# Performance work log

Hardware: AMD Instinct MI355X
Metric: run time of the kernel (lower is better)

Reference implementation:

```python
import jax, jax.numpy as jnp
import numpy as np

B, T, C, H = 4, 2048, 1024, 128

def setup_inputs() -> dict:
    key = jax.random.key(0)
    k1, k2, k3, k4 = jax.random.split(key, 4)
    x = jax.random.normal(k1, (B, T, C), dtype=jnp.float32)
    # nn.Linear(C, H, bias=False) weights, stored as [C, H] so y = x @ W
    scale = 1.0 / np.sqrt(C)
    Wq = jax.random.normal(k2, (C, H), dtype=jnp.float32) * scale
    Wk = jax.random.normal(k3, (C, H), dtype=jnp.float32) * scale
    Wv = jax.random.normal(k4, (C, H), dtype=jnp.float32) * scale
    mask = jnp.tril(jnp.ones((T, T), dtype=jnp.int32))  # causal mask
    return {"x": x, "Wq": Wq, "Wk": Wk, "Wv": Wv, "mask": mask}

def reference(x, Wq, Wk, Wv, mask):
    # x: [B,T,C]; projections to [B,T,H]
    q = jnp.einsum("btc,ch->bth", x, Wq)
    k = jnp.einsum("btc,ch->bth", x, Wk)
    v = jnp.einsum("btc,ch->bth", x, Wv)
    # NOTE: original scales by C**-0.5 (embedding dim), not head_size**-0.5
    inv_scale = x.shape[-1] ** (-0.5)
    scores = jnp.einsum("bth,bsh->bts", q, k) * inv_scale  # [B,T,T]
    scores = jnp.where(mask == 0, -jnp.inf, scores)
    weights = jax.nn.softmax(scores, axis=-1)
    # Dropout(0.1) is identity in eval mode
    return jnp.einsum("bts,bsh->bth", weights, v)  # [B,T,H]
```

## Files before the change

kernel.cpp:

```cpp
#include <hip/hip_runtime.h>
#include <hip/hip_bf16.h>
#include <cstdint>


typedef __bf16 bf16_t;
typedef __bf16 bf16x4 __attribute__((ext_vector_type(4)));
typedef __bf16 bf16x8 __attribute__((ext_vector_type(8)));
typedef float f32x4 __attribute__((ext_vector_type(4)));

#define MFMA16(a, b, c) __builtin_amdgcn_mfma_f32_16x16x32_bf16(a, b, c, 0, 0, 0)

constexpr int T = 2048;
constexpr int C = 1024;
constexpr int H = 128;

__device__ inline bf16x8 load8f(const float* __restrict__ p) {
    float4 a = *(const float4*)p;
    float4 b = *(const float4*)(p + 4);
    bf16x8 r;
    r[0] = (bf16_t)a.x; r[1] = (bf16_t)a.y; r[2] = (bf16_t)a.z; r[3] = (bf16_t)a.w;
    r[4] = (bf16_t)b.x; r[5] = (bf16_t)b.y; r[6] = (bf16_t)b.z; r[7] = (bf16_t)b.w;
    return r;
}

__global__ __launch_bounds__(256) void convert_x(const float* __restrict__ x,
                                                 bf16_t* __restrict__ xb, int n8) {
    int i = blockIdx.x * 256 + threadIdx.x;
    const int stride = gridDim.x * 256;
    for (; i < n8; i += stride)
        *(bf16x8*)(xb + (size_t)i * 8) = load8f(x + (size_t)i * 8);
}

__global__ void transpose_w(const float* __restrict__ Wq,
                            const float* __restrict__ Wk,
                            const float* __restrict__ Wv,
                            bf16_t* __restrict__ Wt) {
    __shared__ bf16_t tile[32][34];
    const float* W = blockIdx.z == 0 ? Wq : (blockIdx.z == 1 ? Wk : Wv);
    const int c0 = blockIdx.x * 32, h0 = blockIdx.y * 32;
    const int tx = threadIdx.x, ty = threadIdx.y;
#pragma unroll
    for (int i = 0; i < 4; i++)
        tile[ty + 8 * i][tx] = (bf16_t)W[(size_t)(c0 + ty + 8 * i) * H + h0 + tx];
    __syncthreads();
    bf16_t* Wtz = Wt + (size_t)blockIdx.z * H * C;
#pragma unroll
    for (int i = 0; i < 4; i++)
        Wtz[(size_t)(h0 + ty + 8 * i) * C + c0 + tx] = tile[tx][ty + 8 * i];
}

__global__ __launch_bounds__(256) void proj_gemm(const bf16_t* __restrict__ xb,
                                                 const bf16_t* __restrict__ Wt,
                                                 bf16_t* __restrict__ qout,
                                                 bf16_t* __restrict__ kout,
                                                 bf16_t* __restrict__ vtout) {
    const int w = threadIdx.x >> 6;
    const int wm = w & 1, wn = w >> 1;
    const int lane = threadIdx.x & 63;
    const int m16 = lane & 15, g = lane >> 4;
    const int z = blockIdx.z;
    const int m0 = blockIdx.x * 64 + wm * 32;
    const int n0 = blockIdx.y * 64 + wn * 32;

    const bf16_t* a0p = xb + (size_t)(m0 + m16) * C + g * 8;
    const bf16_t* a1p = a0p + (size_t)16 * C;
    const bf16_t* b0p = Wt + (size_t)(z * H + n0 + m16) * C + g * 8;
    const bf16_t* b1p = b0p + (size_t)16 * C;

    f32x4 zero = {0.f, 0.f, 0.f, 0.f};
    f32x4 acc00 = zero, acc01 = zero, acc10 = zero, acc11 = zero;

    bf16x8 pa0[4], pa1[4], pb0[4], pb1[4];
#pragma unroll
    for (int j = 0; j < 4; j++) {
        pa0[j] = *(const bf16x8*)(a0p + j * 32);
        pa1[j] = *(const bf16x8*)(a1p + j * 32);
        pb0[j] = *(const bf16x8*)(b0p + j * 32);
        pb1[j] = *(const bf16x8*)(b1p + j * 32);
    }

#pragma unroll
    for (int j = 0; j < C / 32; j++) {
        const int s = j & 3;
        acc00 = MFMA16(pa0[s], pb0[s], acc00);
        acc01 = MFMA16(pa0[s], pb1[s], acc01);
        acc10 = MFMA16(pa1[s], pb0[s], acc10);
        acc11 = MFMA16(pa1[s], pb1[s], acc11);
        const int kn = (j + 4) * 32;
        if (kn < C) {
            pa0[s] = *(const bf16x8*)(a0p + kn);
            pa1[s] = *(const bf16x8*)(a1p + kn);
            pb0[s] = *(const bf16x8*)(b0p + kn);
            pb1[s] = *(const bf16x8*)(b1p + kn);
        }
    }

    const float sc = (z == 0) ? 0.03125f : 1.0f;
    f32x4 acc[2][2] = {{acc00 * sc, acc01 * sc}, {acc10 * sc, acc11 * sc}};

    if (z < 2) {
        bf16_t* out = (z == 0) ? qout : kout;
#pragma unroll
        for (int mf = 0; mf < 2; mf++)
#pragma unroll
            for (int nf = 0; nf < 2; nf++)
#pragma unroll
                for (int ri = 0; ri < 4; ri++) {
                    int r = m0 + mf * 16 + g * 4 + ri;
                    out[(size_t)r * H + n0 + nf * 16 + m16] = (bf16_t)acc[mf][nf][ri];
                }
    } else {
#pragma unroll
        for (int mf = 0; mf < 2; mf++) {
            const int t0 = m0 + mf * 16 + g * 4;
            const int bidx = t0 >> 11, t = t0 & (T - 1);
#pragma unroll
            for (int nf = 0; nf < 2; nf++) {
                const int h = n0 + nf * 16 + m16;
                bf16x4 v;
#pragma unroll
                for (int ri = 0; ri < 4; ri++) v[ri] = (bf16_t)acc[mf][nf][ri];
                *(bf16x4*)(vtout + ((size_t)bidx * H + h) * T + t) = v;
            }
        }
    }
}

__global__ __launch_bounds__(256) void attn(const bf16_t* __restrict__ q,
                                            const bf16_t* __restrict__ k,
                                            const bf16_t* __restrict__ vt,
                                            float* __restrict__ out) {
    __shared__ float accw[4][16][128];
    __shared__ __align__(16) bf16_t pbuf[4][16][40];
    __shared__ float mred[4][16], lred[4][16];
    const int w = threadIdx.x >> 6;
    const int lane = threadIdx.x & 63;
    const int m16 = lane & 15, g = lane >> 4;
    const int b = blockIdx.x & 3;
    const int kk = blockIdx.x >> 2;
    const int qt = (kk < 64) ? kk : 191 - kk;
    const int q0 = qt * 16;

    const bf16_t* qb = q + (size_t)b * T * H;
    const bf16_t* kb = k + (size_t)b * T * H;
    const bf16_t* vb = vt + (size_t)b * H * T;

    bf16x8 aq[4];
#pragma unroll
    for (int c = 0; c < 4; c++)
        aq[c] = *(const bf16x8*)(qb + (size_t)(q0 + m16) * H + c * 32 + g * 8);

    bf16x8 ones;
#pragma unroll
    for (int j = 0; j < 8; j++) ones[j] = (bf16_t)1.0f;

    f32x4 zero = {0.f, 0.f, 0.f, 0.f};
    f32x4 acc[9];
#pragma unroll
    for (int ht = 0; ht < 9; ht++) acc[ht] = zero;
    float mst[4];
#pragma unroll
    for (int ri = 0; ri < 4; ri++) mst[ri] = -1e30f;

    const int kv_end = q0 + 16;
    bf16x8 kc[8], kn[8], vc[8];
    int kv0 = w * 32;
    if (kv0 < kv_end) {
#pragma unroll
        for (int t = 0; t < 2; t++)
#pragma unroll
            for (int c = 0; c < 4; c++)
                kc[t * 4 + c] = *(const bf16x8*)(kb + (size_t)(kv0 + t * 16 + m16) * H + c * 32 + g * 8);
    }

    for (; kv0 < kv_end; kv0 += 128) {
        f32x4 s[2];
        s[0] = zero; s[1] = zero;
#pragma unroll
        for (int t = 0; t < 2; t++)
#pragma unroll
            for (int c = 0; c < 4; c++)
                s[t] = MFMA16(aq[c], kc[t * 4 + c], s[t]);

#pragma unroll
        for (int ht = 0; ht < 8; ht++)
            vc[ht] = *(const bf16x8*)(vb + (size_t)(ht * 16 + m16) * T + kv0 + g * 8);

        const int kvn = kv0 + 128;
        if (kvn < kv_end) {
#pragma unroll
            for (int t = 0; t < 2; t++)
#pragma unroll
                for (int c = 0; c < 4; c++)
                    kn[t * 4 + c] = *(const bf16x8*)(kb + (size_t)(kvn + t * 16 + m16) * H + c * 32 + g * 8);
        }

        float p0v[4], p1v[4];
#pragma unroll
        for (int ri = 0; ri < 4; ri++) {
            const int row = q0 + g * 4 + ri;
            float v0 = s[0][ri];
            float v1 = s[1][ri];
            if (kv0 + m16 > row) v0 = -1e30f;
            if (kv0 + 16 + m16 > row) v1 = -1e30f;
            float rm = fmaxf(v0, v1);
#pragma unroll
            for (int off = 1; off < 16; off <<= 1) rm = fmaxf(rm, __shfl_xor(rm, off));
            const float mnew = fmaxf(mst[ri], rm);
            const float alpha = __expf(mst[ri] - mnew);
            mst[ri] = mnew;
            p0v[ri] = __expf(v0 - mnew);
            p1v[ri] = __expf(v1 - mnew);
#pragma unroll
            for (int ht = 0; ht < 9; ht++) acc[ht][ri] *= alpha;
        }

#pragma unroll
        for (int ri = 0; ri < 4; ri++) {
            pbuf[w][g * 4 + ri][m16] = (bf16_t)p0v[ri];
            pbuf[w][g * 4 + ri][16 + m16] = (bf16_t)p1v[ri];
        }
        bf16x8 ap = *(const bf16x8*)(&pbuf[w][m16][g * 8]);

#pragma unroll
        for (int ht = 0; ht < 8; ht++)
            acc[ht] = MFMA16(ap, vc[ht], acc[ht]);
        acc[8] = MFMA16(ap, ones, acc[8]);

#pragma unroll
        for (int i = 0; i < 8; i++) kc[i] = kn[i];
    }

    if (m16 == 0) {
#pragma unroll
        for (int ri = 0; ri < 4; ri++) mred[w][g * 4 + ri] = mst[ri];
    }
    __syncthreads();
    float scale[4];
#pragma unroll
    for (int ri = 0; ri < 4; ri++) {
        const int row = g * 4 + ri;
        float mt = fmaxf(fmaxf(mred[0][row], mred[1][row]),
                         fmaxf(mred[2][row], mred[3][row]));
        scale[ri] = __expf(mst[ri] - mt);
    }
    if (m16 == 0) {
#pragma unroll
        for (int ri = 0; ri < 4; ri++) lred[w][g * 4 + ri] = acc[8][ri] * scale[ri];
    }
#pragma unroll
    for (int ht = 0; ht < 8; ht++)
#pragma unroll
        for (int ri = 0; ri < 4; ri++)
            accw[w][g * 4 + ri][ht * 16 + m16] = acc[ht][ri] * scale[ri];
    __syncthreads();

    float* ob = out + ((size_t)b * T + q0) * H;
    for (int e = threadIdx.x; e < 16 * 128; e += 256) {
        const int row = e >> 7, col = e & 127;
        float o = accw[0][row][col] + accw[1][row][col] +
                  accw[2][row][col] + accw[3][row][col];
        float l = lred[0][row] + lred[1][row] + lred[2][row] + lred[3][row];
        ob[(size_t)row * H + col] = o / l;
    }
}

extern "C" void kernel_launch(void* const* d_in, const int* in_sizes, int n_in,
                              void* d_out, int out_size, void* d_ws, size_t ws_size,
                              hipStream_t stream) {
    const float* x = (const float*)d_in[0];
    const float* Wq = (const float*)d_in[1];
    const float* Wk = (const float*)d_in[2];
    const float* Wv = (const float*)d_in[3];
    float* out = (float*)d_out;

    char* ws = (char*)d_ws;
    bf16_t* xb = (bf16_t*)ws;
    bf16_t* Wt = (bf16_t*)(ws + 16777216);
    char* p = ws + 16777216 + 786432;
    bf16_t* qb = (bf16_t*)(p);
    bf16_t* kb = (bf16_t*)(p + 2097152);
    bf16_t* vt = (bf16_t*)(p + 2 * 2097152);

    hipLaunchKernelGGL(convert_x, dim3(2048), dim3(256), 0, stream,
                       x, xb, (int)((size_t)4 * T * C / 8));
    hipLaunchKernelGGL(transpose_w, dim3(C / 32, H / 32, 3), dim3(32, 8), 0, stream,
                       Wq, Wk, Wv, Wt);
    hipLaunchKernelGGL(proj_gemm, dim3(128, 2, 3), dim3(256), 0, stream,
                       xb, Wt, qb, kb, vt);
    hipLaunchKernelGGL(attn, dim3(512), dim3(256), 0, stream,
                       qb, kb, vt, out);
}
```

Measured before the change: 170.6 us.

## Stage projection GEMM tiles in LDS via direct global-to-LDS loads; merge prep kernels

The projection GEMM now stages 64-row A tiles and full 128-column B tiles through double-buffered shared memory, filled with global_load_lds and an XOR swizzle. Each block computes all 128 output columns for one of Q/K/V, so the grid drops to 128x3 blocks and operand reuse goes up. The x conversion and weight transpose kernels are folded into one launch to save a launch. The risks are lower occupancy from the larger LDS footprint and fewer blocks, plus a __syncthreads per K step.

```diff
diff --git a/kernel.cpp b/kernel.cpp
--- a/kernel.cpp
+++ b/kernel.cpp
@@ -13,6 +13,7 @@
 constexpr int T = 2048;
 constexpr int C = 1024;
 constexpr int H = 128;
+constexpr int BK = 64;
 
 __device__ inline bf16x8 load8f(const float* __restrict__ p) {
     float4 a = *(const float4*)p;
@@ -23,30 +24,40 @@
     return r;
 }
 
-__global__ __launch_bounds__(256) void convert_x(const float* __restrict__ x,
-                                                 bf16_t* __restrict__ xb, int n8) {
-    int i = blockIdx.x * 256 + threadIdx.x;
-    const int stride = gridDim.x * 256;
-    for (; i < n8; i += stride)
-        *(bf16x8*)(xb + (size_t)i * 8) = load8f(x + (size_t)i * 8);
-}
-
-__global__ void transpose_w(const float* __restrict__ Wq,
-                            const float* __restrict__ Wk,
-                            const float* __restrict__ Wv,
-                            bf16_t* __restrict__ Wt) {
-    __shared__ bf16_t tile[32][34];
-    const float* W = blockIdx.z == 0 ? Wq : (blockIdx.z == 1 ? Wk : Wv);
-    const int c0 = blockIdx.x * 32, h0 = blockIdx.y * 32;
-    const int tx = threadIdx.x, ty = threadIdx.y;
-#pragma unroll
-    for (int i = 0; i < 4; i++)
-        tile[ty + 8 * i][tx] = (bf16_t)W[(size_t)(c0 + ty + 8 * i) * H + h0 + tx];
-    __syncthreads();
-    bf16_t* Wtz = Wt + (size_t)blockIdx.z * H * C;
-#pragma unroll
-    for (int i = 0; i < 4; i++)
-        Wtz[(size_t)(h0 + ty + 8 * i) * C + c0 + tx] = tile[tx][ty + 8 * i];
+__device__ inline void gld16(const bf16_t* g, bf16_t* l) {
+    __builtin_amdgcn_global_load_lds(
+        (const __attribute__((address_space(1))) unsigned int*)g,
+        (__attribute__((address_space(3))) unsigned int*)l, 16, 0, 0);
+}
+
+__global__ __launch_bounds__(256) void prep(const float* __restrict__ x,
+                                            const float* __restrict__ Wq,
+                                            const float* __restrict__ Wk,
+                                            const float* __restrict__ Wv,
+                                            bf16_t* __restrict__ xb,
+                                            bf16_t* __restrict__ Wt) {
+    const int t = threadIdx.x;
+    if (blockIdx.x < 2048) {
+        const int n8 = 4 * T * C / 8;
+        int i = blockIdx.x * 256 + t;
+        for (; i < n8; i += 2048 * 256)
+            *(bf16x8*)(xb + (size_t)i * 8) = load8f(x + (size_t)i * 8);
+    } else {
+        __shared__ bf16_t tile[32][34];
+        const int b2 = blockIdx.x - 2048;
+        const int z = b2 >> 7, rem = b2 & 127;
+        const int c0 = (rem & 31) * 32, h0 = (rem >> 5) * 32;
+        const float* W = z == 0 ? Wq : (z == 1 ? Wk : Wv);
+        const int tx = t & 31, ty = t >> 5;
+#pragma unroll
+        for (int i = 0; i < 4; i++)
+            tile[ty + 8 * i][tx] = (bf16_t)W[(size_t)(c0 + ty + 8 * i) * H + h0 + tx];
+        __syncthreads();
+        bf16_t* Wtz = Wt + (size_t)z * H * C;
+#pragma unroll
+        for (int i = 0; i < 4; i++)
+            Wtz[(size_t)(h0 + ty + 8 * i) * C + c0 + tx] = tile[tx][ty + 8 * i];
+    }
 }
 
 __global__ __launch_bounds__(256) void proj_gemm(const bf16_t* __restrict__ xb,
@@ -54,73 +65,97 @@
                                                  bf16_t* __restrict__ qout,
                                                  bf16_t* __restrict__ kout,
                                                  bf16_t* __restrict__ vtout) {
-    const int w = threadIdx.x >> 6;
+    __shared__ __align__(16) bf16_t Ab[2][64 * BK];
+    __shared__ __align__(16) bf16_t Bb[2][128 * BK];
+    const int t = threadIdx.x;
+    const int w = t >> 6, lane = t & 63;
+    const int m16 = lane & 15, g = lane >> 4;
     const int wm = w & 1, wn = w >> 1;
-    const int lane = threadIdx.x & 63;
-    const int m16 = lane & 15, g = lane >> 4;
-    const int z = blockIdx.z;
-    const int m0 = blockIdx.x * 64 + wm * 32;
-    const int n0 = blockIdx.y * 64 + wn * 32;
-
-    const bf16_t* a0p = xb + (size_t)(m0 + m16) * C + g * 8;
-    const bf16_t* a1p = a0p + (size_t)16 * C;
-    const bf16_t* b0p = Wt + (size_t)(z * H + n0 + m16) * C + g * 8;
-    const bf16_t* b1p = b0p + (size_t)16 * C;
+    const int z = blockIdx.y;
+    const int m0 = blockIdx.x * 64;
+    const bf16_t* Bsrc = Wt + (size_t)z * H * C;
+
+    auto stage = [&](int s, int k0) {
+#pragma unroll
+        for (int i = 0; i < 2; i++) {
+            const int e = i * 256 + t;
+            const int r = e >> 3, v = e & 7, c8 = v ^ (r & 7);
+            gld16(xb + (size_t)(m0 + r) * C + k0 + c8 * 8,
+                  &Ab[s][(i * 4 + w) * 512]);
+        }
+#pragma unroll
+        for (int i = 0; i < 4; i++) {
+            const int e = i * 256 + t;
+            const int r = e >> 3, v = e & 7, c8 = v ^ (r & 7);
+            gld16(Bsrc + (size_t)r * C + k0 + c8 * 8,
+                  &Bb[s][(i * 4 + w) * 512]);
+        }
+    };
 
     f32x4 zero = {0.f, 0.f, 0.f, 0.f};
-    f32x4 acc00 = zero, acc01 = zero, acc10 = zero, acc11 = zero;
-
-    bf16x8 pa0[4], pa1[4], pb0[4], pb1[4];
-#pragma unroll
-    for (int j = 0; j < 4; j++) {
-        pa0[j] = *(const bf16x8*)(a0p + j * 32);
-        pa1[j] = *(const bf16x8*)(a1p + j * 32);
-        pb0[j] = *(const bf16x8*)(b0p + j * 32);
-        pb1[j] = *(const bf16x8*)(b1p + j * 32);
-    }
-
-#pragma unroll
-    for (int j = 0; j < C / 32; j++) {
-        const int s = j & 3;
-        acc00 = MFMA16(pa0[s], pb0[s], acc00);
-        acc01 = MFMA16(pa0[s], pb1[s], acc01);
-        acc10 = MFMA16(pa1[s], pb0[s], acc10);
-        acc11 = MFMA16(pa1[s], pb1[s], acc11);
-        const int kn = (j + 4) * 32;
-        if (kn < C) {
-            pa0[s] = *(const bf16x8*)(a0p + kn);
-            pa1[s] = *(const bf16x8*)(a1p + kn);
-            pb0[s] = *(const bf16x8*)(b0p + kn);
-            pb1[s] = *(const bf16x8*)(b1p + kn);
-        }
+    f32x4 acc[2][4];
+#pragma unroll
+    for (int mf = 0; mf < 2; mf++)
+#pragma unroll
+        for (int nf = 0; nf < 4; nf++) acc[mf][nf] = zero;
+
+    stage(0, 0);
+    for (int c = 0; c < C / BK; c++) {
+        __syncthreads();
+        if (c + 1 < C / BK) stage((c + 1) & 1, (c + 1) * BK);
+        const int s = c & 1;
+
+        bf16x8 af[2][2], bfr[4][2];
+#pragma unroll
+        for (int mf = 0; mf < 2; mf++)
+#pragma unroll
+            for (int kf = 0; kf < 2; kf++) {
+                const int r = wm * 32 + mf * 16 + m16;
+                const int v = (kf * 4 + g) ^ (r & 7);
+                af[mf][kf] = *(const bf16x8*)(&Ab[s][r * BK + v * 8]);
+            }
+#pragma unroll
+        for (int nf = 0; nf < 4; nf++)
+#pragma unroll
+            for (int kf = 0; kf < 2; kf++) {
+                const int r = wn * 64 + nf * 16 + m16;
+                const int v = (kf * 4 + g) ^ (r & 7);
+                bfr[nf][kf] = *(const bf16x8*)(&Bb[s][r * BK + v * 8]);
+            }
+#pragma unroll
+        for (int kf = 0; kf < 2; kf++)
+#pragma unroll
+            for (int mf = 0; mf < 2; mf++)
+#pragma unroll
+                for (int nf = 0; nf < 4; nf++)
+                    acc[mf][nf] = MFMA16(af[mf][kf], bfr[nf][kf], acc[mf][nf]);
     }
 
     const float sc = (z == 0) ? 0.03125f : 1.0f;
-    f32x4 acc[2][2] = {{acc00 * sc, acc01 * sc}, {acc10 * sc, acc11 * sc}};
-
     if (z < 2) {
         bf16_t* out = (z == 0) ? qout : kout;
 #pragma unroll
         for (int mf = 0; mf < 2; mf++)
 #pragma unroll
-            for (int nf = 0; nf < 2; nf++)
+            for (int nf = 0; nf < 4; nf++)
 #pragma unroll
                 for (int ri = 0; ri < 4; ri++) {
-                    int r = m0 + mf * 16 + g * 4 + ri;
-                    out[(size_t)r * H + n0 + nf * 16 + m16] = (bf16_t)acc[mf][nf][ri];
+                    const int r = m0 + wm * 32 + mf * 16 + g * 4 + ri;
+                    const int n = wn * 64 + nf * 16 + m16;
+                    out[(size_t)r * H + n] = (bf16_t)(acc[mf][nf][ri] * sc);
                 }
     } else {
 #pragma unroll
         for (int mf = 0; mf < 2; mf++) {
-            const int t0 = m0 + mf * 16 + g * 4;
-            const int bidx = t0 >> 11, t = t0 & (T - 1);
-#pragma unroll
-            for (int nf = 0; nf < 2; nf++) {
-                const int h = n0 + nf * 16 + m16;
-                bf16x4 v;
-#pragma unroll
-                for (int ri = 0; ri < 4; ri++) v[ri] = (bf16_t)acc[mf][nf][ri];
-                *(bf16x4*)(vtout + ((size_t)bidx * H + h) * T + t) = v;
+            const int t0 = m0 + wm * 32 + mf * 16 + g * 4;
+            const int bidx = t0 >> 11, tt = t0 & (T - 1);
+#pragma unroll
+            for (int nf = 0; nf < 4; nf++) {
+                const int h = wn * 64 + nf * 16 + m16;
+                bf16x4 vv;
+#pragma unroll
+                for (int ri = 0; ri < 4; ri++) vv[ri] = (bf16_t)acc[mf][nf][ri];
+                *(bf16x4*)(vtout + ((size_t)bidx * H + h) * T + tt) = vv;
             }
         }
     }
@@ -282,11 +317,9 @@
     bf16_t* kb = (bf16_t*)(p + 2097152);
     bf16_t* vt = (bf16_t*)(p + 2 * 2097152);
 
-    hipLaunchKernelGGL(convert_x, dim3(2048), dim3(256), 0, stream,
-                       x, xb, (int)((size_t)4 * T * C / 8));
-    hipLaunchKernelGGL(transpose_w, dim3(C / 32, H / 32, 3), dim3(32, 8), 0, stream,
-                       Wq, Wk, Wv, Wt);
-    hipLaunchKernelGGL(proj_gemm, dim3(128, 2, 3), dim3(256), 0, stream,
+    hipLaunchKernelGGL(prep, dim3(2048 + 384), dim3(256), 0, stream,
+                       x, Wq, Wk, Wv, xb, Wt);
+    hipLaunchKernelGGL(proj_gemm, dim3(128, 3), dim3(256), 0, stream,
                        xb, Wt, qb, kb, vt);
     hipLaunchKernelGGL(attn, dim3(512), dim3(256), 0, stream,
                        qb, kb, vt, out);
```

After: 140.7 us. 1.21x faster.
